# Performance work log

Measured on AMD Instinct MI355X. Metric: run time of the kernel, lower is better.

Reference implementation:

```python
import jax, jax.numpy as jnp
from jax import lax
import numpy as np

B, F, H, W, D = 256, 64, 64, 64, 256  # batch, features_dim, map H, map W, input_dim
HC = 32  # hidden conv channels


def setup_inputs() -> dict:
    key = jax.random.key(0)
    ks = jax.random.split(key, 10)
    s = 0.02
    return {
        "x": jax.random.normal(ks[0], (B, D), jnp.float32),
        "state": jax.random.normal(ks[1], (B, F, H, W), jnp.float32),
        "index": jax.random.randint(ks[2], (B, 2), 0, H),
        "conv1_w": jax.random.normal(ks[3], (HC, F, 3, 3), jnp.float32) * s,
        "conv1_b": jnp.zeros((HC,), jnp.float32),
        "conv2_w": jax.random.normal(ks[4], (HC, HC, 3, 3), jnp.float32) * s,
        "conv2_b": jnp.zeros((HC,), jnp.float32),
        "conv3_w": jax.random.normal(ks[5], (HC, HC, 3, 3), jnp.float32) * s,
        "conv3_b": jnp.zeros((HC,), jnp.float32),
        "lin_w": jax.random.normal(ks[6], (HC * H * W, F), jnp.float32) * s,
        "lin_b": jnp.zeros((F,), jnp.float32),
        "write_w": jax.random.normal(ks[7], (D + 2 * F, F), jnp.float32) * s,
        "write_b": jnp.zeros((F,), jnp.float32),
    }


def _conv_relu(h, w, b):
    y = lax.conv_general_dilated(h, w, (1, 1), "SAME",
                                 dimension_numbers=("NCHW", "OIHW", "NCHW"))
    return jax.nn.relu(y + b[None, :, None, None])


def reference(x, state, index, conv1_w, conv1_b, conv2_w, conv2_b,
              conv3_w, conv3_b, lin_w, lin_b, write_w, write_b):
    h = _conv_relu(state, conv1_w, conv1_b)
    h = _conv_relu(h, conv2_w, conv2_b)
    h = _conv_relu(h, conv3_w, conv3_b)
    r = jax.nn.relu(h.reshape(B, -1) @ lin_w + lin_b)  # [B, F]
    # write: gather per-batch map cell, single Linear (MLP with no hidden layers)
    bidx = jnp.arange(B)
    m = state[bidx, :, index[:, 0], index[:, 1]]  # [B, F] gather
    w = jnp.concatenate([x, r, m], axis=1) @ write_w + write_b  # [B, F]
    # scatter updated feature vector back into the state map
    new_state = state.at[bidx, :, index[:, 0], index[:, 1]].set(w)
    return jnp.concatenate([r, w], axis=1), new_state
```

## Files before the change

kernel.cpp:

```cpp
#include <hip/hip_runtime.h>
#include <hip/hip_bf16.h>


typedef __attribute__((ext_vector_type(8))) short bf16x8;
typedef __attribute__((ext_vector_type(4))) float f32x4;

__device__ inline unsigned short f2bfu(float f) {
    __hip_bfloat16 h = __float2bfloat16(f);
    return *reinterpret_cast<unsigned short*>(&h);
}

__global__ __launch_bounds__(256)
void repack_w_k(const float* __restrict__ w1, const float* __restrict__ w2,
                const float* __restrict__ w3, __hip_bfloat16* __restrict__ rw)
{
    int idx = blockIdx.x * 256 + threadIdx.x;
    const float* src; int CIN, li;
    if (idx < 18432)      { src = w1; CIN = 64; li = idx; }
    else if (idx < 27648) { src = w2; CIN = 32; li = idx - 18432; }
    else                  { src = w3; CIN = 32; li = idx - 27648; }
    int ci = li & 31;
    int co = (li >> 5) & 31;
    int t2 = li >> 10;
    int ks = t2 % 9;
    int ch = t2 / 9;
    rw[idx] = __float2bfloat16(src[((size_t)(co * CIN + ch * 32 + ci)) * 9 + ks]);
}

__global__ __launch_bounds__(256)
void nchw_to_nhwc_k(const float* __restrict__ in,
                    __hip_bfloat16* __restrict__ outp)
{
    __shared__ unsigned short s[64][72];
    const int blk = blockIdx.x;
    const int b = blk >> 6, y = blk & 63;
    const int t = threadIdx.x;

    const float* src = in + (size_t)b * 262144 + (size_t)y * 64;
    #pragma unroll
    for (int q = 0; q < 4; ++q) {
        int c = q * 16 + (t >> 4);
        int x = (t & 15) * 4;
        float4 v = *(const float4*)(src + (size_t)c * 4096 + x);
        *(ushort4*)&s[c][x] = make_ushort4(f2bfu(v.x), f2bfu(v.y), f2bfu(v.z), f2bfu(v.w));
    }
    __syncthreads();

    __hip_bfloat16* dst = outp + ((size_t)b * 4096 + y * 64) * 64;
    #pragma unroll
    for (int q = 0; q < 4; ++q) {
        int x = q * 16 + (t >> 4);
        int c = (t & 15) * 4;
        ushort4 o = make_ushort4(s[c + 0][x], s[c + 1][x], s[c + 2][x], s[c + 3][x]);
        *(ushort4*)(dst + (size_t)x * 64 + c) = o;
    }
}

template<int CIN>
__global__ __launch_bounds__(256, 3)
void conv_mfma_k(const __hip_bfloat16* __restrict__ in,
                 const __hip_bfloat16* __restrict__ rw,
                 const float* __restrict__ bias,
                 __hip_bfloat16* __restrict__ out)
{
    constexpr int NCH = CIN / 32;
    __shared__ __hip_bfloat16 s_in[18 * 34 * 40];

    const int b    = blockIdx.x;
    const int ty0  = (blockIdx.y >> 1) * 16;
    const int tx0  = (blockIdx.y & 1) * 32;
    const int t    = threadIdx.x;
    const int lane = t & 63;
    const int wv   = t >> 6;
    const int ln   = lane & 15;
    const int lg   = lane >> 4;

    const f32x4 zero4 = {0.f, 0.f, 0.f, 0.f};
    f32x4 acc[8][2];
    #pragma unroll
    for (int p = 0; p < 8; ++p) { acc[p][0] = zero4; acc[p][1] = zero4; }

    int bbase[8];
    #pragma unroll
    for (int p = 0; p < 8; ++p) {
        int gg = wv * 8 + p;
        bbase[p] = (((gg >> 1) * 34) + (gg & 1) * 16 + ln) * 80 + lg * 16;
    }

    for (int ch = 0; ch < NCH; ++ch) {
        bf16x8 wf[9][2];
        #pragma unroll
        for (int ks = 0; ks < 9; ++ks)
            #pragma unroll
            for (int cg = 0; cg < 2; ++cg)
                wf[ks][cg] = *(const bf16x8*)(rw + ((size_t)((ch * 9 + ks) * 32 + cg * 16 + ln)) * 32 + lg * 8);

        uint4 vreg[10];
        #pragma unroll
        for (int q = 0; q < 10; ++q) {
            int id = q * 256 + t;
            uint4 v = make_uint4(0u, 0u, 0u, 0u);
            if (id < 2448) {
                int c8 = id & 3, px = id >> 2;
                int ly = px / 34, lx = px - ly * 34;
                int gy = ty0 - 1 + ly, gx = tx0 - 1 + lx;
                if ((unsigned)gy < 64u && (unsigned)gx < 64u)
                    v = *(const uint4*)(in + ((size_t)b * 4096 + gy * 64 + gx) * CIN + ch * 32 + c8 * 8);
            }
            vreg[q] = v;
        }
        #pragma unroll
        for (int q = 0; q < 10; ++q) {
            int id = q * 256 + t;
            if (id < 2448) {
                int c8 = id & 3, px = id >> 2;
                *(uint4*)(reinterpret_cast<char*>(s_in) + px * 80 + c8 * 16) = vreg[q];
            }
        }
        __syncthreads();

        #pragma unroll
        for (int ky = 0; ky < 3; ++ky)
        #pragma unroll
        for (int kx = 0; kx < 3; ++kx) {
            const int ks   = ky * 3 + kx;
            const int koff = (ky * 34 + kx) * 80;
            #pragma unroll
            for (int p = 0; p < 8; ++p) {
                bf16x8 bfr = *(const bf16x8*)(reinterpret_cast<const char*>(s_in) + bbase[p] + koff);
                acc[p][0] = __builtin_amdgcn_mfma_f32_16x16x32_bf16(wf[ks][0], bfr, acc[p][0], 0, 0, 0);
                acc[p][1] = __builtin_amdgcn_mfma_f32_16x16x32_bf16(wf[ks][1], bfr, acc[p][1], 0, 0, 0);
            }
        }
        __syncthreads();
    }

    #pragma unroll
    for (int p = 0; p < 8; ++p) {
        int gg = wv * 8 + p;
        int y  = ty0 + (gg >> 1);
        int x  = tx0 + (gg & 1) * 16 + ln;
        size_t pxb = ((size_t)b * 4096 + y * 64 + x) * 32;
        #pragma unroll
        for (int cg = 0; cg < 2; ++cg) {
            int co0 = cg * 16 + lg * 4;
            float4 bv = *(const float4*)(bias + co0);
            ushort4 o;
            o.x = f2bfu(fmaxf(acc[p][cg][0] + bv.x, 0.f));
            o.y = f2bfu(fmaxf(acc[p][cg][1] + bv.y, 0.f));
            o.z = f2bfu(fmaxf(acc[p][cg][2] + bv.z, 0.f));
            o.w = f2bfu(fmaxf(acc[p][cg][3] + bv.w, 0.f));
            *(ushort4*)(out + pxb + co0) = o;
        }
    }
}

__global__ __launch_bounds__(256)
void lin_partial_k(const __hip_bfloat16* __restrict__ h3,
                   const float* __restrict__ lw,
                   float* __restrict__ partial)
{
    __shared__ float s_h[32][260];
    __shared__ float s_w[32][64];
    const int t  = threadIdx.x;
    const int k0 = blockIdx.x * 512;
    const int f0 = (t & 15) * 4;
    const int b0 = (t >> 4) * 16;

    float acc[16][4];
    #pragma unroll
    for (int i = 0; i < 16; ++i)
        #pragma unroll
        for (int j = 0; j < 4; ++j) acc[i][j] = 0.f;

    for (int kk = 0; kk < 512; kk += 32) {
        #pragma unroll
        for (int i = 0; i < 8; ++i) {
            int id = i * 256 + t;
            int bb = id >> 3;
            int pc = id & 7;
            ushort4 hv = *(const ushort4*)(h3 + (size_t)bb * 131072 + k0 + kk + pc * 4);
            s_h[pc * 4 + 0][bb] = __uint_as_float((unsigned)hv.x << 16);
            s_h[pc * 4 + 1][bb] = __uint_as_float((unsigned)hv.y << 16);
            s_h[pc * 4 + 2][bb] = __uint_as_float((unsigned)hv.z << 16);
            s_h[pc * 4 + 3][bb] = __uint_as_float((unsigned)hv.w << 16);
        }
        #pragma unroll
        for (int i = 0; i < 2; ++i) {
            int id = i * 256 + t;
            int kr = id >> 4;
            int c4 = (id & 15) * 4;
            int k  = k0 + kk + kr;
            size_t ref = (size_t)(k & 31) * 4096 + (size_t)(k >> 5);
            float4 wv = *(const float4*)&lw[ref * 64 + c4];
            *(float4*)&s_w[kr][c4] = wv;
        }
        __syncthreads();
        for (int k = 0; k < 32; ++k) {
            float4 wv = *(const float4*)&s_w[k][f0];
            #pragma unroll
            for (int ii = 0; ii < 4; ++ii) {
                float4 hv = *(const float4*)&s_h[k][b0 + ii * 4];
                float hvv[4] = {hv.x, hv.y, hv.z, hv.w};
                #pragma unroll
                for (int l = 0; l < 4; ++l) {
                    acc[ii * 4 + l][0] += hvv[l] * wv.x;
                    acc[ii * 4 + l][1] += hvv[l] * wv.y;
                    acc[ii * 4 + l][2] += hvv[l] * wv.z;
                    acc[ii * 4 + l][3] += hvv[l] * wv.w;
                }
            }
        }
        __syncthreads();
    }

    float* pp = partial + (size_t)blockIdx.x * 16384;
    #pragma unroll
    for (int i = 0; i < 16; ++i) {
        float4 v = make_float4(acc[i][0], acc[i][1], acc[i][2], acc[i][3]);
        *(float4*)&pp[(b0 + i) * 64 + f0] = v;
    }
}

__global__ __launch_bounds__(256)
void lin_reduce_k(const float* __restrict__ partial,
                  const float* __restrict__ lb,
                  float* __restrict__ out)
{
    int idx = blockIdx.x * 256 + threadIdx.x;
    int b = idx >> 6, f = idx & 63;
    float s = lb[f];
    for (int c = 0; c < 256; ++c) s += partial[(size_t)c * 16384 + idx];
    out[(size_t)b * 128 + f] = fmaxf(s, 0.f);
}

__global__ __launch_bounds__(256)
void write_k(const float* __restrict__ x,
             const float* __restrict__ state,
             const int* __restrict__ index,
             const float* __restrict__ ww,
             const float* __restrict__ wb,
             float* __restrict__ out)
{
    int idx = blockIdx.x * 256 + threadIdx.x;
    int b = idx >> 6, f = idx & 63;
    int i0 = index[b * 2 + 0];
    int i1 = index[b * 2 + 1];
    float s = wb[f];
    for (int k = 0; k < 256; ++k) s += x[(size_t)b * 256 + k] * ww[k * 64 + f];
    for (int k = 0; k < 64; ++k)  s += out[(size_t)b * 128 + k] * ww[(256 + k) * 64 + f];
    const float* mp = state + (size_t)b * 262144 + (size_t)i0 * 64 + i1;
    for (int k = 0; k < 64; ++k)  s += mp[(size_t)k * 4096] * ww[(320 + k) * 64 + f];
    out[(size_t)b * 128 + 64 + f] = s;
}

__global__ __launch_bounds__(256)
void copy_state_k(const float4* __restrict__ src, float4* __restrict__ dst, int n4)
{
    int stride = gridDim.x * blockDim.x;
    for (int i = blockIdx.x * blockDim.x + threadIdx.x; i < n4; i += stride)
        dst[i] = src[i];
}

__global__ __launch_bounds__(256)
void scatter_k(const int* __restrict__ index,
               const float* __restrict__ out_ro,
               float* __restrict__ ns)
{
    int idx = blockIdx.x * 256 + threadIdx.x;
    int b = idx >> 6, f = idx & 63;
    int i0 = index[b * 2 + 0];
    int i1 = index[b * 2 + 1];
    ns[(((size_t)b * 64 + f) * 64 + i0) * 64 + i1] = out_ro[(size_t)b * 128 + 64 + f];
}

extern "C" void kernel_launch(void* const* d_in, const int* in_sizes, int n_in,
                              void* d_out, int out_size, void* d_ws, size_t ws_size,
                              hipStream_t stream)
{
    (void)in_sizes; (void)n_in; (void)out_size; (void)d_ws; (void)ws_size;
    const float* x     = (const float*)d_in[0];
    const float* state = (const float*)d_in[1];
    const int*   idx   = (const int*)d_in[2];
    const float* c1w   = (const float*)d_in[3];
    const float* c1b   = (const float*)d_in[4];
    const float* c2w   = (const float*)d_in[5];
    const float* c2b   = (const float*)d_in[6];
    const float* c3w   = (const float*)d_in[7];
    const float* c3b   = (const float*)d_in[8];
    const float* lw    = (const float*)d_in[9];
    const float* lb    = (const float*)d_in[10];
    const float* ww    = (const float*)d_in[11];
    const float* wb    = (const float*)d_in[12];

    float* out = (float*)d_out;
    float* ns  = out + 32768;

    __hip_bfloat16* rw  = (__hip_bfloat16*)out;
    __hip_bfloat16* rw1 = rw;
    __hip_bfloat16* rw2 = rw + 18432;
    __hip_bfloat16* rw3 = rw + 27648;

    __hip_bfloat16* h1    = (__hip_bfloat16*)ns;
    __hip_bfloat16* h2    = h1 + 33554432;
    __hip_bfloat16* h3    = h1;
    __hip_bfloat16* snhwc = (__hip_bfloat16*)(ns + 33554432);
    float* partial        = (float*)h2;

    repack_w_k    <<<144, 256, 0, stream>>>(c1w, c2w, c3w, rw);
    nchw_to_nhwc_k<<<16384, 256, 0, stream>>>(state, snhwc);
    conv_mfma_k<64><<<dim3(256, 8), 256, 0, stream>>>(snhwc, rw1, c1b, h1);
    conv_mfma_k<32><<<dim3(256, 8), 256, 0, stream>>>(h1, rw2, c2b, h2);
    conv_mfma_k<32><<<dim3(256, 8), 256, 0, stream>>>(h2, rw3, c3b, h3);
    lin_partial_k<<<256, 256, 0, stream>>>(h3, lw, partial);
    lin_reduce_k <<<64, 256, 0, stream>>>(partial, lb, out);
    write_k      <<<64, 256, 0, stream>>>(x, state, idx, ww, wb, out);
    copy_state_k <<<8192, 256, 0, stream>>>((const float4*)state, (float4*)ns, 16777216);
    scatter_k    <<<64, 256, 0, stream>>>(idx, out, ns);
}
```

Before: 846.2 us.

## Fuse state copy into transpose and merge tail kernels using workspace

When a large enough workspace is supplied, scratch buffers move out of the output state region into the workspace. The state copy can then be folded into the NCHW-to-NHWC transpose kernel, so the state is read from memory once instead of twice. The linear reduce, write-MLP and scatter kernels are merged into one tail kernel to cut launches and intermediate traffic. Without enough workspace the old path runs unchanged, so whether the new path is used depends on the harness-provided workspace size.

```diff
diff --git a/kernel.cpp b/kernel.cpp
--- a/kernel.cpp
+++ b/kernel.cpp
@@ -25,6 +25,38 @@
     int ks = t2 % 9;
     int ch = t2 / 9;
     rw[idx] = __float2bfloat16(src[((size_t)(co * CIN + ch * 32 + ci)) * 9 + ks]);
+}
+
+__global__ __launch_bounds__(256)
+void copy_transpose_k(const float* __restrict__ in,
+                      float* __restrict__ nsd,
+                      __hip_bfloat16* __restrict__ outp)
+{
+    __shared__ unsigned short s[64][72];
+    const int blk = blockIdx.x;
+    const int b = blk >> 6, y = blk & 63;
+    const int t = threadIdx.x;
+
+    const float* src = in  + (size_t)b * 262144 + (size_t)y * 64;
+    float*       dst = nsd + (size_t)b * 262144 + (size_t)y * 64;
+    #pragma unroll
+    for (int q = 0; q < 4; ++q) {
+        int c = q * 16 + (t >> 4);
+        int x = (t & 15) * 4;
+        float4 v = *(const float4*)(src + (size_t)c * 4096 + x);
+        *(float4*)(dst + (size_t)c * 4096 + x) = v;
+        *(ushort4*)&s[c][x] = make_ushort4(f2bfu(v.x), f2bfu(v.y), f2bfu(v.z), f2bfu(v.w));
+    }
+    __syncthreads();
+
+    __hip_bfloat16* dq = outp + ((size_t)b * 4096 + y * 64) * 64;
+    #pragma unroll
+    for (int q = 0; q < 4; ++q) {
+        int x = q * 16 + (t >> 4);
+        int c = (t & 15) * 4;
+        ushort4 o = make_ushort4(s[c + 0][x], s[c + 1][x], s[c + 2][x], s[c + 3][x]);
+        *(ushort4*)(dq + (size_t)x * 64 + c) = o;
+    }
 }
 
 __global__ __launch_bounds__(256)
@@ -223,6 +255,43 @@
 }
 
 __global__ __launch_bounds__(256)
+void tail_k(const float* __restrict__ partial,
+            const float* __restrict__ lb,
+            const float* __restrict__ x,
+            const float* __restrict__ state,
+            const int* __restrict__ index,
+            const float* __restrict__ ww,
+            const float* __restrict__ wb,
+            float* __restrict__ out,
+            float* __restrict__ ns)
+{
+    __shared__ float r_s[4][64];
+    const int t  = threadIdx.x;
+    const int bl = t >> 6;
+    const int f  = t & 63;
+    const int b  = blockIdx.x * 4 + bl;
+
+    float s = lb[f];
+    const float* pp = partial + (size_t)b * 64 + f;
+    for (int c = 0; c < 256; ++c) s += pp[(size_t)c * 16384];
+    float r = fmaxf(s, 0.f);
+    out[(size_t)b * 128 + f] = r;
+    r_s[bl][f] = r;
+    __syncthreads();
+
+    int i0 = index[b * 2 + 0];
+    int i1 = index[b * 2 + 1];
+    float w = wb[f];
+    const float* xb = x + (size_t)b * 256;
+    for (int k = 0; k < 256; ++k) w += xb[k] * ww[k * 64 + f];
+    for (int k = 0; k < 64; ++k)  w += r_s[bl][k] * ww[(256 + k) * 64 + f];
+    const float* mp = state + (size_t)b * 262144 + (size_t)i0 * 64 + i1;
+    for (int k = 0; k < 64; ++k)  w += mp[(size_t)k * 4096] * ww[(320 + k) * 64 + f];
+    out[(size_t)b * 128 + 64 + f] = w;
+    ns[(((size_t)b * 64 + f) * 64 + i0) * 64 + i1] = w;
+}
+
+__global__ __launch_bounds__(256)
 void lin_reduce_k(const float* __restrict__ partial,
                   const float* __restrict__ lb,
                   float* __restrict__ out)
@@ -278,7 +347,7 @@
                               void* d_out, int out_size, void* d_ws, size_t ws_size,
                               hipStream_t stream)
 {
-    (void)in_sizes; (void)n_in; (void)out_size; (void)d_ws; (void)ws_size;
+    (void)in_sizes; (void)n_in; (void)out_size;
     const float* x     = (const float*)d_in[0];
     const float* state = (const float*)d_in[1];
     const int*   idx   = (const int*)d_in[2];
@@ -301,20 +370,37 @@
     __hip_bfloat16* rw2 = rw + 18432;
     __hip_bfloat16* rw3 = rw + 27648;
 
-    __hip_bfloat16* h1    = (__hip_bfloat16*)ns;
-    __hip_bfloat16* h2    = h1 + 33554432;
-    __hip_bfloat16* h3    = h1;
-    __hip_bfloat16* snhwc = (__hip_bfloat16*)(ns + 33554432);
-    float* partial        = (float*)h2;
-
-    repack_w_k    <<<144, 256, 0, stream>>>(c1w, c2w, c3w, rw);
-    nchw_to_nhwc_k<<<16384, 256, 0, stream>>>(state, snhwc);
-    conv_mfma_k<64><<<dim3(256, 8), 256, 0, stream>>>(snhwc, rw1, c1b, h1);
-    conv_mfma_k<32><<<dim3(256, 8), 256, 0, stream>>>(h1, rw2, c2b, h2);
-    conv_mfma_k<32><<<dim3(256, 8), 256, 0, stream>>>(h2, rw3, c3b, h3);
-    lin_partial_k<<<256, 256, 0, stream>>>(h3, lw, partial);
-    lin_reduce_k <<<64, 256, 0, stream>>>(partial, lb, out);
-    write_k      <<<64, 256, 0, stream>>>(x, state, idx, ww, wb, out);
-    copy_state_k <<<8192, 256, 0, stream>>>((const float4*)state, (float4*)ns, 16777216);
-    scatter_k    <<<64, 256, 0, stream>>>(idx, out, ns);
-}
+    const size_t WS_NEED = 268435456;
+    if (d_ws != nullptr && ws_size >= WS_NEED) {
+        __hip_bfloat16* snhwc = (__hip_bfloat16*)d_ws;
+        __hip_bfloat16* h1    = snhwc + 67108864;
+        __hip_bfloat16* h2    = h1 + 33554432;
+        __hip_bfloat16* h3    = h1;
+        float* partial        = (float*)h2;
+
+        repack_w_k      <<<144, 256, 0, stream>>>(c1w, c2w, c3w, rw);
+        copy_transpose_k<<<16384, 256, 0, stream>>>(state, ns, snhwc);
+        conv_mfma_k<64> <<<dim3(256, 8), 256, 0, stream>>>(snhwc, rw1, c1b, h1);
+        conv_mfma_k<32> <<<dim3(256, 8), 256, 0, stream>>>(h1, rw2, c2b, h2);
+        conv_mfma_k<32> <<<dim3(256, 8), 256, 0, stream>>>(h2, rw3, c3b, h3);
+        lin_partial_k   <<<256, 256, 0, stream>>>(h3, lw, partial);
+        tail_k          <<<64, 256, 0, stream>>>(partial, lb, x, state, idx, ww, wb, out, ns);
+    } else {
+        __hip_bfloat16* h1    = (__hip_bfloat16*)ns;
+        __hip_bfloat16* h2    = h1 + 33554432;
+        __hip_bfloat16* h3    = h1;
+        __hip_bfloat16* snhwc = (__hip_bfloat16*)(ns + 33554432);
+        float* partial        = (float*)h2;
+
+        repack_w_k    <<<144, 256, 0, stream>>>(c1w, c2w, c3w, rw);
+        nchw_to_nhwc_k<<<16384, 256, 0, stream>>>(state, snhwc);
+        conv_mfma_k<64><<<dim3(256, 8), 256, 0, stream>>>(snhwc, rw1, c1b, h1);
+        conv_mfma_k<32><<<dim3(256, 8), 256, 0, stream>>>(h1, rw2, c2b, h2);
+        conv_mfma_k<32><<<dim3(256, 8), 256, 0, stream>>>(h2, rw3, c3b, h3);
+        lin_partial_k<<<256, 256, 0, stream>>>(h3, lw, partial);
+        lin_reduce_k <<<64, 256, 0, stream>>>(partial, lb, out);
+        write_k      <<<64, 256, 0, stream>>>(x, state, idx, ww, wb, out);
+        copy_state_k <<<8192, 256, 0, stream>>>((const float4*)state, (float4*)ns, 16777216);
+        scatter_k    <<<64, 256, 0, stream>>>(idx, out, ns);
+    }
+}
```

New measurement: 778.4 us. -8.0%, faster.
